# Kernel optimization log

Measured on AMD Instinct MI355X. Metric: run time of the kernel, lower is better.

Reference implementation:

```python
import jax, jax.numpy as jnp
import numpy as np

N = 32768        # num_nodes
D = 256          # hidden_dim
H = 8            # num_heads
DH = D // H      # head_dim
S = 4            # num_scales
CS = max(3, N // 10)          # cluster size (pos=None path)
C = (N + CS - 1) // CS        # num_clusters
EPS = 1e-5


def setup_inputs() -> dict:
    key = jax.random.key(0)
    ks = jax.random.split(key, 16)
    w = 0.02
    return {
        "x": jax.random.normal(ks[0], (N, D), dtype=jnp.float32),
        "edge_index": jax.random.randint(ks[1], (2, 16 * N), 0, N),
        "batch": jnp.zeros((N,), dtype=jnp.int32),
        # per-scale AttentionPooling params (stacked over S)
        "Wk": jax.random.normal(ks[2], (S, D, D), dtype=jnp.float32) * w,
        "bk": jnp.zeros((S, D), dtype=jnp.float32),
        "Wv": jax.random.normal(ks[3], (S, D, D), dtype=jnp.float32) * w,
        "bv": jnp.zeros((S, D), dtype=jnp.float32),
        "Wo": jax.random.normal(ks[4], (S, D, D), dtype=jnp.float32) * w,
        "bo": jnp.zeros((S, D), dtype=jnp.float32),
        "pool_query": jax.random.normal(ks[5], (S, H, DH), dtype=jnp.float32),
        # scale fusion params
        "Wf1": jax.random.normal(ks[6], (S * D, D), dtype=jnp.float32) * w,
        "bf1": jnp.zeros((D,), dtype=jnp.float32),
        "ln_g": jnp.ones((D,), dtype=jnp.float32),
        "ln_b": jnp.zeros((D,), dtype=jnp.float32),
        "Wf2": jax.random.normal(ks[7], (D, D), dtype=jnp.float32) * w,
        "bf2": jnp.zeros((D,), dtype=jnp.float32),
    }


def reference(x, edge_index, batch, Wk, bk, Wv, bv, Wo, bo, pool_query,
              Wf1, bf1, ln_g, ln_b, Wf2, bf2):
    # clusters from pos=None branch: arange(N) // cluster_size (same at all scales)
    clusters = jnp.arange(N) // CS                                  # [N]
    scale = DH ** -0.5

    # all S scales vectorized (params stacked on axis s)
    keys = (jnp.einsum('nd,sde->nse', x, Wk) + bk).reshape(N, S, H, DH)
    values = (jnp.einsum('nd,sde->nse', x, Wv) + bv).reshape(N, S, H, DH)

    # pool_query is identical for every node -> scores[n,s,h] = <k, q> * scale
    scores = jnp.einsum('nshd,shd->nsh', keys, pool_query) * scale  # [N,S,H]

    # per-cluster softmax over the node dim (segment softmax)
    smax = jax.ops.segment_max(scores, clusters, num_segments=C)    # [C,S,H]
    ex = jnp.exp(scores - smax[clusters])
    denom = jax.ops.segment_sum(ex, clusters, num_segments=C)
    weights = ex / denom[clusters]                                  # [N,S,H]

    # attended values, scatter-mean over clusters
    attended = (weights[..., None] * values).reshape(N, S, D)       # [N,S,D]
    counts = jax.ops.segment_sum(jnp.ones((N,), dtype=x.dtype), clusters, num_segments=C)
    pooled = jax.ops.segment_sum(attended, clusters, num_segments=C) / counts[:, None, None]

    # out_proj then gather back to nodes
    out = jnp.einsum('csd,sde->cse', pooled, Wo) + bo               # [C,S,D]
    node = out[clusters]                                            # [N,S,D]

    # scale fusion: Linear -> LayerNorm -> GELU -> (Dropout eval=id) -> Linear
    combined = node.reshape(N, S * D)
    h = combined @ Wf1 + bf1
    mu = jnp.mean(h, axis=-1, keepdims=True)
    var = jnp.mean(jnp.square(h - mu), axis=-1, keepdims=True)
    h = (h - mu) / jnp.sqrt(var + EPS) * ln_g + ln_b
    h = jax.nn.gelu(h, approximate=False)
    fused = h @ Wf2 + bf2                                           # [N,D]
    return fused
```

## Files before the change

kernel.cpp:

```cpp
#include <hip/hip_runtime.h>
#include <math.h>


namespace {
constexpr int N   = 32768;
constexpr int CS  = 3276;
constexpr int CPC = 52;
constexpr int NB  = CPC*10 + 1;

constexpr size_t CQ_OFF   = 0;
constexpr size_t WQBF_OFF = 32;
constexpr size_t PART_OFF = WQBF_OFF + 4096;
constexpr size_t PS_OFF   = PART_OFF + (size_t)NB*8192;
constexpr size_t XW_OFF   = PS_OFF + 352;
constexpr size_t PL_OFF   = XW_OFF + 90112;
constexpr size_t OL_OFF   = PL_OFF + 11264;
constexpr size_t HP_OFF   = OL_OFF + 11264;
constexpr size_t FP_OFF   = HP_OFF + 11264;
}

typedef __attribute__((ext_vector_type(8))) short short8;
typedef __attribute__((ext_vector_type(4))) float f32x4;

__device__ __forceinline__ unsigned f2bf(float f){
  unsigned u = __float_as_uint(f);
  unsigned r = u + 0x7FFFu + ((u >> 16) & 1u);
  return r >> 16;
}

__global__ __launch_bounds__(256) void ka(const float* __restrict__ Wk, const float* __restrict__ bk,
                                          const float* __restrict__ pq, float* __restrict__ ws){
  int b = blockIdx.x, t = threadIdx.x;
  const float scale = 0.17677669529663688f;
  if (b < 32){
    __shared__ float row[256];
    int s = b >> 3, h = b & 7;
    const float* wrow = Wk + ((size_t)s<<16) + (size_t)t*256 + h*32;
    const float* q = pq + (s*8 + h)*32;
    float a = 0.f;
#pragma unroll
    for (int j=0;j<32;j++) a = fmaf(wrow[j], q[j], a);
    row[t] = a*scale;
    __syncthreads();
    if (t < 32){
      int ks = t & 7, kg2 = t >> 3;
      const float* src = row + ks*32 + kg2*8;
      uint4 p;
      p.x = f2bf(src[0]) | (f2bf(src[1]) << 16);
      p.y = f2bf(src[2]) | (f2bf(src[3]) << 16);
      p.z = f2bf(src[4]) | (f2bf(src[5]) << 16);
      p.w = f2bf(src[6]) | (f2bf(src[7]) << 16);
      int Nt = b >> 4, l15b = b & 15;
      ((uint4*)(ws + WQBF_OFF))[(size_t)(Nt*8 + ks)*64 + l15b + 16*kg2] = p;
    }
  } else {
    if (t < 32){
      int s = t >> 3, h = t & 7;
      const float* br = bk + s*256 + h*32;
      const float* q = pq + t*32;
      float a = 0.f;
#pragma unroll
      for (int j=0;j<32;j++) a = fmaf(br[j], q[j], a);
      ws[CQ_OFF + t] = a*scale;
    }
    for (int i = t; i < 352; i += 256) ws[PS_OFF + i] = 0.f;
  }
}

__global__ __launch_bounds__(512,4) void kbd10(const float* __restrict__ x, float* __restrict__ ws){
  int b = blockIdx.x, t = threadIdx.x;
  int c  = (b < 520) ? (b / CPC) : 10;
  int wi = (b < 520) ? (b % CPC) : 0;
  int n0 = c*CS + wi*64;
  int n1 = min(n0 + 64, min((c+1)*CS, N));
  int cnt = n1 - n0;

  __shared__ __align__(16) unsigned short xtb[64*264];
  __shared__ __align__(16) unsigned short swT[32*72];
  __shared__ float psb[16*32];

  int wv = t >> 6, lane = t & 63;
  int Mt = wv & 3, Nt = wv >> 2;
  int l15 = lane & 15, kg = lane >> 4;
  int arow = Mt*16 + l15;
  uint4 bfr[8];
  const uint4* WQBF4 = (const uint4*)(ws + WQBF_OFF);
#pragma unroll
  for (int ks=0; ks<8; ++ks) bfr[ks] = WQBF4[(size_t)(Nt*8 + ks)*64 + lane];
  float cqv = ws[CQ_OFF + Nt*16 + l15];
  int shc = Nt*16 + l15;

  const float4* X4 = (const float4*)x;
#pragma unroll
  for (int k=0;k<8;k++){
    int f = t + k*512;
    int j = f >> 6, c4 = f & 63;
    float4 v = (n0 + j < N) ? X4[(size_t)(n0+j)*64 + c4] : make_float4(0.f,0.f,0.f,0.f);
    uint2 p;
    p.x = f2bf(v.x) | (f2bf(v.y) << 16);
    p.y = f2bf(v.z) | (f2bf(v.w) << 16);
    *(uint2*)(xtb + j*264 + c4*4) = p;
  }
  __syncthreads();

  f32x4 acc1 = {0.f, 0.f, 0.f, 0.f};
#pragma unroll
  for (int ks=0; ks<8; ++ks){
    union { uint4 q; short8 v; } A, B;
    A.q = *(const uint4*)(xtb + arow*264 + ks*32 + kg*8);
    B.q = bfr[ks];
    acc1 = __builtin_amdgcn_mfma_f32_16x16x32_bf16(A.v, B.v, acc1, 0, 0, 0);
  }
  {
    float ev[4];
    float s4 = 0.f;
#pragma unroll
    for (int r=0;r<4;r++){
      int jl = Mt*16 + kg*4 + r;
      float e = (jl < cnt) ? __expf(acc1[r] + cqv) : 0.f;
      ev[r] = e; s4 += e;
    }
    uint2 wp;
    wp.x = f2bf(ev[0]) | (f2bf(ev[1]) << 16);
    wp.y = f2bf(ev[2]) | (f2bf(ev[3]) << 16);
    *(uint2*)(swT + (size_t)shc*72 + Mt*16 + kg*4) = wp;
    psb[(Mt*4 + kg)*32 + shc] = s4;
  }
  __syncthreads();
  if (t < 32){
    float S = 0.f;
#pragma unroll
    for (int k=0;k<16;k++) S += psb[k*32 + t];
    unsafeAtomicAdd(ws + PS_OFF + (size_t)c*32 + t, S);
  }

  int Mt2 = wv & 1, Nq = wv >> 1;
  union FR { uint4 q; short8 v; };
  FR a0, a1;
  a0.q = *(const uint4*)(swT + (size_t)(Mt2*16 + l15)*72 + kg*8);
  a1.q = *(const uint4*)(swT + (size_t)(Mt2*16 + l15)*72 + 32 + kg*8);
  unsigned xb = (unsigned)(size_t)&xtb[0];
  unsigned va = xb + (unsigned)(kg*4224 + (l15>>2)*528 + (l15&3)*8 + Nq*128);
  unsigned long long tr[4][2][2];
#pragma unroll
  for (int i=0;i<4;i++){
#pragma unroll
    for (int k2=0;k2<2;k2++){
      asm volatile("ds_read_b64_tr_b16 %0, %2 offset:%c3\n\t"
                   "ds_read_b64_tr_b16 %1, %2 offset:%c4"
                   : "=v"(tr[i][k2][0]), "=v"(tr[i][k2][1])
                   : "v"(va), "i"(i*32 + k2*16896), "i"(i*32 + k2*16896 + 2112));
    }
  }
  asm volatile("s_waitcnt lgkmcnt(0)" ::: "memory");
  __builtin_amdgcn_sched_barrier(0);
  f32x4 o[4] = {{0.f,0.f,0.f,0.f},{0.f,0.f,0.f,0.f},{0.f,0.f,0.f,0.f},{0.f,0.f,0.f,0.f}};
#pragma unroll
  for (int i=0;i<4;i++){
#pragma unroll
    for (int k2=0;k2<2;k2++){
      FR Bf;
      Bf.q.x = (unsigned)(tr[i][k2][0] & 0xffffffffULL);
      Bf.q.y = (unsigned)(tr[i][k2][0] >> 32);
      Bf.q.z = (unsigned)(tr[i][k2][1] & 0xffffffffULL);
      Bf.q.w = (unsigned)(tr[i][k2][1] >> 32);
      o[i] = __builtin_amdgcn_mfma_f32_16x16x32_bf16(k2 ? a1.v : a0.v, Bf.v, o[i], 0, 0, 0);
    }
  }
  float* pr = ws + PART_OFF + (size_t)b*8192;
#pragma unroll
  for (int i=0;i<4;i++){
    int dcol = Nq*64 + i*16 + l15;
#pragma unroll
    for (int r=0;r<4;r++)
      pr[(size_t)(Mt2*16 + kg*4 + r)*256 + dcol] = o[i][r];
  }
}

__global__ __launch_bounds__(256) void ke2(float* __restrict__ ws){
  int b = blockIdx.x, t = threadIdx.x;
  int c = b >> 5, sh = b & 31;
  int nch = (c < 10) ? CPC : 1;
  int cb  = (c < 10) ? c*CPC : 520;
  float rden = 1.0f / ws[PS_OFF + (size_t)c*32 + sh];
  const float* part = ws + PART_OFF + (size_t)sh*256 + t;
  float a = 0.f;
  for (int k=0;k<nch;k++) a += part[(size_t)(cb+k)*8192];
  ws[XW_OFF + (size_t)c*8192 + (size_t)sh*256 + t] = a * rden;
}

__global__ __launch_bounds__(256) void kp(float* __restrict__ ws,
    const float* __restrict__ Wv, const float* __restrict__ bv){
  int b = blockIdx.x; int c = b >> 4, rem = b & 15, s = rem >> 2, eq = rem & 3;
  int t = threadIdx.x, e64 = t & 63, dq = t >> 6;
  int e = eq*64 + e64, h = e >> 5;
  const float* xr = ws + XW_OFF + (size_t)c*8192 + (size_t)(s*8 + h)*256 + dq*64;
  const float* wv = Wv + (size_t)s*65536 + (size_t)(dq*64)*256 + e;
  float a = 0.f;
#pragma unroll 8
  for (int d=0; d<64; ++d) a = fmaf(wv[(size_t)d*256], xr[d], a);
  __shared__ float red[4][64];
  red[dq][e64] = a;
  __syncthreads();
  if (t < 64){
    float rcnt = (c < 10) ? (1.0f/(float)CS) : 0.125f;
    float p = (red[0][t]+red[1][t]+red[2][t]+red[3][t] + bv[s*256 + eq*64 + t]) * rcnt;
    ws[PL_OFF + (size_t)c*1024 + s*256 + eq*64 + t] = p;
  }
}

__global__ __launch_bounds__(256) void ko(float* __restrict__ ws,
    const float* __restrict__ Wo, const float* __restrict__ bo){
  int b = blockIdx.x; int c = b >> 4, rem = b & 15, s = rem >> 2, eq = rem & 3;
  int t = threadIdx.x, e64 = t & 63, dq = t >> 6;
  int e = eq*64 + e64;
  const float* pr = ws + PL_OFF + (size_t)c*1024 + s*256 + dq*64;
  const float* wo = Wo + (size_t)s*65536 + (size_t)(dq*64)*256 + e;
  float a = 0.f;
#pragma unroll 8
  for (int d=0; d<64; ++d) a = fmaf(wo[(size_t)d*256], pr[d], a);
  __shared__ float red[4][64];
  red[dq][e64] = a;
  __syncthreads();
  if (t < 64)
    ws[OL_OFF + (size_t)c*1024 + s*256 + eq*64 + t] =
      red[0][t]+red[1][t]+red[2][t]+red[3][t] + bo[s*256 + eq*64 + t];
}

__global__ __launch_bounds__(256) void kf1(const float* __restrict__ Wf1, float* __restrict__ ws){
  int b = blockIdx.x; int c = b >> 4, fq = (b >> 2) & 3, kq = b & 3;
  int t = threadIdx.x, f64 = t & 63, ks = t >> 6;
  const float* ol = ws + OL_OFF + (size_t)c*1024 + kq*256 + ks*64;
  const float* wf = Wf1 + (size_t)(kq*256 + ks*64)*256 + fq*64 + f64;
  float a = 0.f;
#pragma unroll 8
  for (int i=0; i<64; ++i) a = fmaf(wf[(size_t)i*256], ol[i], a);
  __shared__ float red[4][64];
  red[ks][f64] = a;
  __syncthreads();
  if (t < 64)
    ws[HP_OFF + (size_t)(c*4 + kq)*256 + fq*64 + t] = red[0][t]+red[1][t]+red[2][t]+red[3][t];
}

__global__ __launch_bounds__(256) void kf2b(const float* __restrict__ Wf2, float* __restrict__ ws,
    const float* __restrict__ bf1, const float* __restrict__ lng, const float* __restrict__ lnb){
  int b = blockIdx.x; int c = b >> 4, gq = (b >> 2) & 3, kq = b & 3;
  int t = threadIdx.x;
  __shared__ float hl[256];
  __shared__ float rs1[4], rs2[4];
  float hacc = bf1[t];
#pragma unroll
  for (int q=0;q<4;q++) hacc += ws[HP_OFF + (size_t)(c*4+q)*256 + t];
  float s1 = hacc, s2v = hacc*hacc;
  for (int off=32; off>0; off>>=1){ s1 += __shfl_down(s1, off, 64); s2v += __shfl_down(s2v, off, 64); }
  int wid = t>>6, lane = t&63;
  if (lane==0){ rs1[wid]=s1; rs2[wid]=s2v; }
  __syncthreads();
  float S1 = rs1[0]+rs1[1]+rs1[2]+rs1[3];
  float S2 = rs2[0]+rs2[1]+rs2[2]+rs2[3];
  float mu = S1*(1.0f/256.0f);
  float var = S2*(1.0f/256.0f) - mu*mu;
  float rsig = rsqrtf(var + 1e-5f);
  float hn = (hacc - mu)*rsig*lng[t] + lnb[t];
  hl[t] = 0.5f*hn*(1.0f + erff(hn*0.70710678118654752f));
  __syncthreads();
  int g64 = t & 63, ks = t >> 6;
  const float* hh = hl + kq*64 + ks*16;
  const float* wf = Wf2 + (size_t)(kq*64 + ks*16)*256 + gq*64 + g64;
  float a = 0.f;
#pragma unroll
  for (int i=0; i<16; ++i) a = fmaf(wf[(size_t)i*256], hh[i], a);
  __shared__ float red[4][64];
  red[ks][g64] = a;
  __syncthreads();
  if (t < 64)
    ws[FP_OFF + (size_t)(c*4 + kq)*256 + gq*64 + t] = red[0][t]+red[1][t]+red[2][t]+red[3][t];
}

__global__ __launch_bounds__(256) void kbc2(const float* __restrict__ ws, float4* __restrict__ out,
                                            const float* __restrict__ bf2){
  unsigned bidx = blockIdx.x, t = threadIdx.x;
  unsigned idx = bidx*256u + t;
  unsigned c = (bidx*4u) / (unsigned)CS;
  __shared__ float4 row[64];
  if (t < 64){
    const float4* FP4 = (const float4*)(ws + FP_OFF);
    float4 s0 = FP4[(c*4+0)*64 + t];
    float4 s1 = FP4[(c*4+1)*64 + t];
    float4 s2 = FP4[(c*4+2)*64 + t];
    float4 s3 = FP4[(c*4+3)*64 + t];
    float4 bb = ((const float4*)bf2)[t];
    row[t] = make_float4(s0.x+s1.x+s2.x+s3.x+bb.x, s0.y+s1.y+s2.y+s3.y+bb.y,
                         s0.z+s1.z+s2.z+s3.z+bb.z, s0.w+s1.w+s2.w+s3.w+bb.w);
  }
  __syncthreads();
  out[idx] = row[t & 63u];
}

extern "C" void kernel_launch(void* const* d_in, const int* in_sizes, int n_in,
                              void* d_out, int out_size, void* d_ws, size_t ws_size,
                              hipStream_t stream) {
  const float* x   = (const float*)d_in[0];
  const float* Wk  = (const float*)d_in[3];
  const float* bk  = (const float*)d_in[4];
  const float* Wv  = (const float*)d_in[5];
  const float* bv  = (const float*)d_in[6];
  const float* Wo  = (const float*)d_in[7];
  const float* bo  = (const float*)d_in[8];
  const float* pq  = (const float*)d_in[9];
  const float* Wf1 = (const float*)d_in[10];
  const float* bf1 = (const float*)d_in[11];
  const float* lng = (const float*)d_in[12];
  const float* lnb = (const float*)d_in[13];
  const float* Wf2 = (const float*)d_in[14];
  const float* bf2 = (const float*)d_in[15];
  float* ws = (float*)d_ws;
  float4* out = (float4*)d_out;

  hipLaunchKernelGGL(ka,    dim3(33),   dim3(256), 0, stream, Wk, bk, pq, ws);
  hipLaunchKernelGGL(kbd10, dim3(NB),   dim3(512), 0, stream, x, ws);
  hipLaunchKernelGGL(ke2,   dim3(352),  dim3(256), 0, stream, ws);
  hipLaunchKernelGGL(kp,    dim3(176),  dim3(256), 0, stream, ws, Wv, bv);
  hipLaunchKernelGGL(ko,    dim3(176),  dim3(256), 0, stream, ws, Wo, bo);
  hipLaunchKernelGGL(kf1,   dim3(176),  dim3(256), 0, stream, Wf1, ws);
  hipLaunchKernelGGL(kf2b,  dim3(176),  dim3(256), 0, stream, Wf2, ws, bf1, lng, lnb);
  hipLaunchKernelGGL(kbc2,  dim3(8192), dim3(256), 0, stream, ws, out, bf2);
}
```

Before: 61.76 us.

## Fuse per-cluster projection and fusion-MLP kernels into two large-block kernels

Merges the value projection and the output projection into one kernel with 1024-thread blocks, one block per cluster and scale, with the pooled vector kept in shared memory. Merges Wf1, LayerNorm, GELU and Wf2 into one kernel per cluster that writes the final row with bias, so the broadcast kernel only copies it. This cuts launches from eight to six and removes several workspace round trips. In exchange it uses far fewer blocks (44 and 11), so each chain of dependent FMAs runs on few CUs and the weight-streaming loops are longer per thread.

```diff
diff --git a/kernel.cpp b/kernel.cpp
--- a/kernel.cpp
+++ b/kernel.cpp
@@ -13,10 +13,8 @@
 constexpr size_t PART_OFF = WQBF_OFF + 4096;
 constexpr size_t PS_OFF   = PART_OFF + (size_t)NB*8192;
 constexpr size_t XW_OFF   = PS_OFF + 352;
-constexpr size_t PL_OFF   = XW_OFF + 90112;
-constexpr size_t OL_OFF   = PL_OFF + 11264;
-constexpr size_t HP_OFF   = OL_OFF + 11264;
-constexpr size_t FP_OFF   = HP_OFF + 11264;
+constexpr size_t OL_OFF   = XW_OFF + 90112;
+constexpr size_t CF2_OFF  = OL_OFF + 11264;
 }
 
 typedef __attribute__((ext_vector_type(8))) short short8;
@@ -60,7 +58,7 @@
       const float* q = pq + t*32;
       float a = 0.f;
 #pragma unroll
-      for (int j=0;j<32;j++) a = fmaf(br[j], q[j], a);
+    for (int j=0;j<32;j++) a = fmaf(br[j], q[j], a);
       ws[CQ_OFF + t] = a*scale;
     }
     for (int i = t; i < 352; i += 256) ws[PS_OFF + i] = 0.f;
@@ -189,110 +187,101 @@
   ws[XW_OFF + (size_t)c*8192 + (size_t)sh*256 + t] = a * rden;
 }
 
-__global__ __launch_bounds__(256) void kp(float* __restrict__ ws,
-    const float* __restrict__ Wv, const float* __restrict__ bv){
-  int b = blockIdx.x; int c = b >> 4, rem = b & 15, s = rem >> 2, eq = rem & 3;
-  int t = threadIdx.x, e64 = t & 63, dq = t >> 6;
-  int e = eq*64 + e64, h = e >> 5;
-  const float* xr = ws + XW_OFF + (size_t)c*8192 + (size_t)(s*8 + h)*256 + dq*64;
-  const float* wv = Wv + (size_t)s*65536 + (size_t)(dq*64)*256 + e;
-  float a = 0.f;
+__global__ __launch_bounds__(1024) void kpo2(float* __restrict__ ws,
+    const float* __restrict__ Wv, const float* __restrict__ bv,
+    const float* __restrict__ Wo, const float* __restrict__ bo){
+  int b = blockIdx.x; int c = b >> 2, s = b & 3; int t = threadIdx.x;
+  __shared__ float red[4][256];
+  __shared__ float pl[256];
+  int e = t & 255, dsl = t >> 8;
+  int h = e >> 5;
+  {
+    const float* xr = ws + XW_OFF + (size_t)c*8192 + (size_t)(s*8 + h)*256 + dsl*64;
+    const float* wv = Wv + (size_t)s*65536 + (size_t)(dsl*64)*256 + e;
+    float a = 0.f;
 #pragma unroll 8
-  for (int d=0; d<64; ++d) a = fmaf(wv[(size_t)d*256], xr[d], a);
-  __shared__ float red[4][64];
-  red[dq][e64] = a;
-  __syncthreads();
-  if (t < 64){
+    for (int d=0; d<64; ++d) a = fmaf(wv[(size_t)d*256], xr[d], a);
+    red[dsl][e] = a;
+  }
+  __syncthreads();
+  if (t < 256){
     float rcnt = (c < 10) ? (1.0f/(float)CS) : 0.125f;
-    float p = (red[0][t]+red[1][t]+red[2][t]+red[3][t] + bv[s*256 + eq*64 + t]) * rcnt;
-    ws[PL_OFF + (size_t)c*1024 + s*256 + eq*64 + t] = p;
-  }
-}
-
-__global__ __launch_bounds__(256) void ko(float* __restrict__ ws,
-    const float* __restrict__ Wo, const float* __restrict__ bo){
-  int b = blockIdx.x; int c = b >> 4, rem = b & 15, s = rem >> 2, eq = rem & 3;
-  int t = threadIdx.x, e64 = t & 63, dq = t >> 6;
-  int e = eq*64 + e64;
-  const float* pr = ws + PL_OFF + (size_t)c*1024 + s*256 + dq*64;
-  const float* wo = Wo + (size_t)s*65536 + (size_t)(dq*64)*256 + e;
-  float a = 0.f;
+    pl[t] = (red[0][t]+red[1][t]+red[2][t]+red[3][t] + bv[s*256 + t]) * rcnt;
+  }
+  __syncthreads();
+  {
+    const float* pr = pl + dsl*64;
+    const float* wo = Wo + (size_t)s*65536 + (size_t)(dsl*64)*256 + e;
+    float o = 0.f;
 #pragma unroll 8
-  for (int d=0; d<64; ++d) a = fmaf(wo[(size_t)d*256], pr[d], a);
-  __shared__ float red[4][64];
-  red[dq][e64] = a;
-  __syncthreads();
-  if (t < 64)
-    ws[OL_OFF + (size_t)c*1024 + s*256 + eq*64 + t] =
-      red[0][t]+red[1][t]+red[2][t]+red[3][t] + bo[s*256 + eq*64 + t];
-}
-
-__global__ __launch_bounds__(256) void kf1(const float* __restrict__ Wf1, float* __restrict__ ws){
-  int b = blockIdx.x; int c = b >> 4, fq = (b >> 2) & 3, kq = b & 3;
-  int t = threadIdx.x, f64 = t & 63, ks = t >> 6;
-  const float* ol = ws + OL_OFF + (size_t)c*1024 + kq*256 + ks*64;
-  const float* wf = Wf1 + (size_t)(kq*256 + ks*64)*256 + fq*64 + f64;
-  float a = 0.f;
+    for (int d=0; d<64; ++d) o = fmaf(wo[(size_t)d*256], pr[d], o);
+    red[dsl][e] = o;
+  }
+  __syncthreads();
+  if (t < 256)
+    ws[OL_OFF + (size_t)c*1024 + s*256 + t] = red[0][t]+red[1][t]+red[2][t]+red[3][t] + bo[s*256 + t];
+}
+
+__global__ __launch_bounds__(1024) void kfc(float* __restrict__ ws,
+    const float* __restrict__ Wf1, const float* __restrict__ bf1,
+    const float* __restrict__ lng, const float* __restrict__ lnb,
+    const float* __restrict__ Wf2, const float* __restrict__ bf2){
+  int c = blockIdx.x, t = threadIdx.x;
+  __shared__ float oll[1024];
+  __shared__ float hp[4][256];
+  __shared__ float hl[256];
+  __shared__ float fp[4][256];
+  __shared__ float rs1[4], rs2[4];
+  oll[t] = ws[OL_OFF + (size_t)c*1024 + t];
+  __syncthreads();
+  int f = t & 255, kq = t >> 8;
+  {
+    float a = 0.f;
+    const float* wf = Wf1 + (size_t)(kq*256)*256 + f;
+    const float* ol = oll + kq*256;
 #pragma unroll 8
-  for (int i=0; i<64; ++i) a = fmaf(wf[(size_t)i*256], ol[i], a);
-  __shared__ float red[4][64];
-  red[ks][f64] = a;
-  __syncthreads();
-  if (t < 64)
-    ws[HP_OFF + (size_t)(c*4 + kq)*256 + fq*64 + t] = red[0][t]+red[1][t]+red[2][t]+red[3][t];
-}
-
-__global__ __launch_bounds__(256) void kf2b(const float* __restrict__ Wf2, float* __restrict__ ws,
-    const float* __restrict__ bf1, const float* __restrict__ lng, const float* __restrict__ lnb){
-  int b = blockIdx.x; int c = b >> 4, gq = (b >> 2) & 3, kq = b & 3;
-  int t = threadIdx.x;
-  __shared__ float hl[256];
-  __shared__ float rs1[4], rs2[4];
-  float hacc = bf1[t];
-#pragma unroll
-  for (int q=0;q<4;q++) hacc += ws[HP_OFF + (size_t)(c*4+q)*256 + t];
-  float s1 = hacc, s2v = hacc*hacc;
-  for (int off=32; off>0; off>>=1){ s1 += __shfl_down(s1, off, 64); s2v += __shfl_down(s2v, off, 64); }
-  int wid = t>>6, lane = t&63;
-  if (lane==0){ rs1[wid]=s1; rs2[wid]=s2v; }
-  __syncthreads();
-  float S1 = rs1[0]+rs1[1]+rs1[2]+rs1[3];
-  float S2 = rs2[0]+rs2[1]+rs2[2]+rs2[3];
-  float mu = S1*(1.0f/256.0f);
-  float var = S2*(1.0f/256.0f) - mu*mu;
-  float rsig = rsqrtf(var + 1e-5f);
-  float hn = (hacc - mu)*rsig*lng[t] + lnb[t];
-  hl[t] = 0.5f*hn*(1.0f + erff(hn*0.70710678118654752f));
-  __syncthreads();
-  int g64 = t & 63, ks = t >> 6;
-  const float* hh = hl + kq*64 + ks*16;
-  const float* wf = Wf2 + (size_t)(kq*64 + ks*16)*256 + gq*64 + g64;
-  float a = 0.f;
-#pragma unroll
-  for (int i=0; i<16; ++i) a = fmaf(wf[(size_t)i*256], hh[i], a);
-  __shared__ float red[4][64];
-  red[ks][g64] = a;
-  __syncthreads();
-  if (t < 64)
-    ws[FP_OFF + (size_t)(c*4 + kq)*256 + gq*64 + t] = red[0][t]+red[1][t]+red[2][t]+red[3][t];
-}
-
-__global__ __launch_bounds__(256) void kbc2(const float* __restrict__ ws, float4* __restrict__ out,
-                                            const float* __restrict__ bf2){
+    for (int i=0;i<256;i++) a = fmaf(wf[(size_t)i*256], ol[i], a);
+    hp[kq][f] = a;
+  }
+  __syncthreads();
+  float hacc = 0.f;
+  if (t < 256){
+    hacc = hp[0][t]+hp[1][t]+hp[2][t]+hp[3][t] + bf1[t];
+    float s1 = hacc, s2v = hacc*hacc;
+    for (int off=32; off>0; off>>=1){ s1 += __shfl_down(s1, off, 64); s2v += __shfl_down(s2v, off, 64); }
+    int wid = t>>6, lane = t&63;
+    if (lane==0){ rs1[wid]=s1; rs2[wid]=s2v; }
+  }
+  __syncthreads();
+  if (t < 256){
+    float S1 = rs1[0]+rs1[1]+rs1[2]+rs1[3];
+    float S2 = rs2[0]+rs2[1]+rs2[2]+rs2[3];
+    float mu = S1*(1.0f/256.0f);
+    float var = S2*(1.0f/256.0f) - mu*mu;
+    float rsig = rsqrtf(var + 1e-5f);
+    float hn = (hacc - mu)*rsig*lng[t] + lnb[t];
+    hl[t] = 0.5f*hn*(1.0f + erff(hn*0.70710678118654752f));
+  }
+  __syncthreads();
+  {
+    float a = 0.f;
+    const float* wf = Wf2 + (size_t)(kq*64)*256 + f;
+    const float* hh = hl + kq*64;
+#pragma unroll
+    for (int i=0;i<64;i++) a = fmaf(wf[(size_t)i*256], hh[i], a);
+    fp[kq][f] = a;
+  }
+  __syncthreads();
+  if (t < 256)
+    ws[CF2_OFF + (size_t)c*256 + t] = fp[0][t]+fp[1][t]+fp[2][t]+fp[3][t] + bf2[t];
+}
+
+__global__ __launch_bounds__(256) void kbc3(const float* __restrict__ ws, float4* __restrict__ out){
   unsigned bidx = blockIdx.x, t = threadIdx.x;
   unsigned idx = bidx*256u + t;
   unsigned c = (bidx*4u) / (unsigned)CS;
   __shared__ float4 row[64];
-  if (t < 64){
-    const float4* FP4 = (const float4*)(ws + FP_OFF);
-    float4 s0 = FP4[(c*4+0)*64 + t];
-    float4 s1 = FP4[(c*4+1)*64 + t];
-    float4 s2 = FP4[(c*4+2)*64 + t];
-    float4 s3 = FP4[(c*4+3)*64 + t];
-    float4 bb = ((const float4*)bf2)[t];
-    row[t] = make_float4(s0.x+s1.x+s2.x+s3.x+bb.x, s0.y+s1.y+s2.y+s3.y+bb.y,
-                         s0.z+s1.z+s2.z+s3.z+bb.z, s0.w+s1.w+s2.w+s3.w+bb.w);
-  }
+  if (t < 64) row[t] = ((const float4*)(ws + CF2_OFF))[c*64u + t];
   __syncthreads();
   out[idx] = row[t & 63u];
 }
@@ -317,12 +306,10 @@
   float* ws = (float*)d_ws;
   float4* out = (float4*)d_out;
 
-  hipLaunchKernelGGL(ka,    dim3(33),   dim3(256), 0, stream, Wk, bk, pq, ws);
-  hipLaunchKernelGGL(kbd10, dim3(NB),   dim3(512), 0, stream, x, ws);
-  hipLaunchKernelGGL(ke2,   dim3(352),  dim3(256), 0, stream, ws);
-  hipLaunchKernelGGL(kp,    dim3(176),  dim3(256), 0, stream, ws, Wv, bv);
-  hipLaunchKernelGGL(ko,    dim3(176),  dim3(256), 0, stream, ws, Wo, bo);
-  hipLaunchKernelGGL(kf1,   dim3(176),  dim3(256), 0, stream, Wf1, ws);
-  hipLaunchKernelGGL(kf2b,  dim3(176),  dim3(256), 0, stream, Wf2, ws, bf1, lng, lnb);
-  hipLaunchKernelGGL(kbc2,  dim3(8192), dim3(256), 0, stream, ws, out, bf2);
-}
+  hipLaunchKernelGGL(ka,    dim3(33),   dim3(256),  0, stream, Wk, bk, pq, ws);
+  hipLaunchKernelGGL(kbd10, dim3(NB),   dim3(512),  0, stream, x, ws);
+  hipLaunchKernelGGL(ke2,   dim3(352),  dim3(256),  0, stream, ws);
+  hipLaunchKernelGGL(kpo2,  dim3(44),   dim3(1024), 0, stream, ws, Wv, bv, Wo, bo);
+  hipLaunchKernelGGL(kfc,   dim3(11),   dim3(1024), 0, stream, ws, Wf1, bf1, lng, lnb, Wf2, bf2);
+  hipLaunchKernelGGL(kbc3,  dim3(8192), dim3(256),  0, stream, ws, out);
+}
```

New measurement: 70.07 us. 13.5% more time.
